# Kernel tuning notes

Hardware: AMD Instinct MI355X
Metric: run time of the kernel (lower is better)

## Reference

```python
import jax, jax.numpy as jnp
import numpy as np

E, D, H, N = 600000, 128, 256, 50000
LN_EPS = 1e-5


def layer_norm(x, g, b):
    mu = jnp.mean(x, axis=-1, keepdims=True)
    var = jnp.var(x, axis=-1, keepdims=True)
    return (x - mu) * jax.lax.rsqrt(var + LN_EPS) * g + b


def setup_inputs() -> dict:
    key = jax.random.key(0)
    ks = jax.random.split(key, 8)
    edges = jax.random.normal(ks[0], (E, D), dtype=jnp.float32)
    edges_index = jax.random.randint(ks[1], (E,), 0, N, dtype=jnp.int64)
    # params (PyTorch Linear default-ish init scale)
    w1 = jax.random.normal(ks[2], (D, H), dtype=jnp.float32) * (1.0 / np.sqrt(D))
    b1 = jnp.zeros((H,), dtype=jnp.float32)
    w2 = jax.random.normal(ks[3], (H, H), dtype=jnp.float32) * (1.0 / np.sqrt(H))
    b2 = jnp.zeros((H,), dtype=jnp.float32)
    wg = jax.random.normal(ks[4], (H, 1), dtype=jnp.float32) * (1.0 / np.sqrt(H))
    bg = jnp.zeros((1,), dtype=jnp.float32)
    wo = jax.random.normal(ks[5], (H, D), dtype=jnp.float32) * (1.0 / np.sqrt(H))
    bo = jnp.zeros((D,), dtype=jnp.float32)
    return {
        "edges": edges, "edges_index": edges_index, "num_nodes": N,
        "ln1_g": jnp.ones((D,), jnp.float32), "ln1_b": jnp.zeros((D,), jnp.float32),
        "w1": w1, "b1": b1,
        "ln2_g": jnp.ones((H,), jnp.float32), "ln2_b": jnp.zeros((H,), jnp.float32),
        "w2": w2, "b2": b2,
        "wg": wg, "bg": bg,
        "wo": wo, "bo": bo,
    }


def reference(edges, edges_index, num_nodes, ln1_g, ln1_b, w1, b1, ln2_g, ln2_b, w2, b2, wg, bg, wo, bo):
    # edge MLP: LN -> Linear -> ELU -> LN -> Linear
    h = layer_norm(edges, ln1_g, ln1_b)
    h = jax.nn.elu(h @ w1 + b1)
    h = layer_norm(h, ln2_g, ln2_b)
    h = h @ w2 + b2                      # [E, H]
    # gated output projection
    gate = jax.nn.sigmoid(h @ wg + bg)   # [E, 1]
    out = (h @ wo + bo) * gate           # [E, D]
    # scatter_add over destination nodes
    res = jax.ops.segment_sum(out, edges_index, num_segments=num_nodes)  # [N, D]
    return res
```

## Files before the change

### kernel.cpp

```cpp
#include <hip/hip_runtime.h>
#include <hip/hip_bf16.h>

typedef unsigned short u16;
typedef unsigned int u32;
typedef __bf16 bf16x8 __attribute__((ext_vector_type(8)));
typedef float f32x4 __attribute__((ext_vector_type(4)));

#define D 128
#define H 256
#define TM 32
#define THREADS 256
#define LN_EPS 1e-5f

__device__ __forceinline__ u32 f2bf(float f) {
    union { float f; u32 u; } v; v.f = f;
    return (v.u + 0x7FFFu + ((v.u >> 16) & 1u)) >> 16;
}

__global__ void pack_weights(const float* __restrict__ w1,
                             const float* __restrict__ w2,
                             const float* __restrict__ wo,
                             u16* __restrict__ pw) {
    int tid = blockIdx.x * blockDim.x + threadIdx.x;
    const float* W; int K, NN, local;
    if (tid < 32768)       { W = w1; K = 128; NN = 256; local = tid; }
    else if (tid < 98304)  { W = w2; K = 256; NN = 256; local = tid - 32768; }
    else if (tid < 131072) { W = wo; K = 256; NN = 128; local = tid - 98304; }
    else return;
    int b = local >> 9, within = local & 511;
    int l = within >> 3, i = within & 7;
    int nbk = K >> 5;
    int n0 = (b / nbk) << 4, k0 = (b % nbk) << 5;
    int k = k0 + ((l >> 4) << 3) + i;
    int n = n0 + (l & 15);
    pw[tid] = (u16)f2bf(W[k * NN + n]);
}

__global__ void zero_out_kernel(float4* __restrict__ out, int n4) {
    int i = blockIdx.x * blockDim.x + threadIdx.x;
    if (i < n4) out[i] = float4{0.f, 0.f, 0.f, 0.f};
}

__global__ __launch_bounds__(THREADS, 3) void fused_edge_kernel(
    const float* __restrict__ edges, const int* __restrict__ eidx,
    const float* __restrict__ ln1_g, const float* __restrict__ ln1_b,
    const float* __restrict__ b1,
    const float* __restrict__ ln2_g, const float* __restrict__ ln2_b,
    const float* __restrict__ b2,
    const float* __restrict__ wg, const float* __restrict__ bg,
    const float* __restrict__ bo,
    const u16* __restrict__ pw1, const u16* __restrict__ pw2,
    const u16* __restrict__ pwo,
    float* __restrict__ out, int E)
{
    __shared__ u16 sH[TM * H];
    __shared__ float sRedS[4][TM];
    __shared__ float sRedQ[4][TM];
    __shared__ float sMu[TM], sRs[TM], sGate[TM];
    __shared__ int   sIdx[TM];
    u16* sA = sH;

    const int t    = threadIdx.x;
    const int lane = t & 63;
    const int wave = t >> 6;
    const int lr   = lane & 15;
    const int lg   = lane >> 4;
    const int e0   = blockIdx.x * TM;

    if (t < TM) sIdx[t] = (e0 + t < E) ? eidx[e0 + t] : 0;

    {
        const int row = t >> 3;
        const int c8  = t & 7;
        const int er  = min(e0 + row, E - 1);
        const float* src = edges + (size_t)er * D + c8 * 16;
        float x[16];
        #pragma unroll
        for (int i = 0; i < 4; ++i) {
            float4 v = reinterpret_cast<const float4*>(src)[i];
            x[i*4+0]=v.x; x[i*4+1]=v.y; x[i*4+2]=v.z; x[i*4+3]=v.w;
        }
        float s = 0.f, sq = 0.f;
        #pragma unroll
        for (int i = 0; i < 16; ++i) { s += x[i]; sq += x[i]*x[i]; }
        s  += __shfl_xor(s, 1);  s  += __shfl_xor(s, 2);  s  += __shfl_xor(s, 4);
        sq += __shfl_xor(sq, 1); sq += __shfl_xor(sq, 2); sq += __shfl_xor(sq, 4);
        const float mu  = s * (1.0f / D);
        const float var = sq * (1.0f / D) - mu * mu;
        const float rs  = rsqrtf(var + LN_EPS);
        #pragma unroll
        for (int i = 0; i < 2; ++i) {
            u32 p[4];
            #pragma unroll
            for (int j = 0; j < 4; ++j) {
                int c0 = c8*16 + i*8 + j*2;
                float y0 = (x[i*8+j*2+0] - mu) * rs * ln1_g[c0+0] + ln1_b[c0+0];
                float y1 = (x[i*8+j*2+1] - mu) * rs * ln1_g[c0+1] + ln1_b[c0+1];
                p[j] = f2bf(y0) | (f2bf(y1) << 16);
            }
            int idx = (row * D + c8*16 + i*8) ^ ((row & 7) << 3);
            *reinterpret_cast<uint4*>(&sA[idx]) = uint4{p[0], p[1], p[2], p[3]};
        }
    }
    __syncthreads();

    f32x4 acc[2][4];
    #pragma unroll
    for (int a = 0; a < 2; ++a)
        #pragma unroll
        for (int b = 0; b < 4; ++b) acc[a][b] = f32x4{0.f,0.f,0.f,0.f};

    #pragma unroll
    for (int ks = 0; ks < 4; ++ks) {
        bf16x8 af[2];
        #pragma unroll
        for (int mt = 0; mt < 2; ++mt) {
            int row = mt*16 + lr;
            int idx = (row * D + ks*32 + lg*8) ^ ((row & 7) << 3);
            af[mt] = *reinterpret_cast<const bf16x8*>(&sA[idx]);
        }
        bf16x8 bv[4];
        #pragma unroll
        for (int nt = 0; nt < 4; ++nt) {
            int ctile = wave*4 + nt;
            int blk = ctile * 4 + ks;
            bv[nt] = *reinterpret_cast<const bf16x8*>(pw1 + blk*512 + lane*8);
        }
        #pragma unroll
        for (int mt = 0; mt < 2; ++mt)
            #pragma unroll
            for (int nt = 0; nt < 4; ++nt)
                acc[mt][nt] = __builtin_amdgcn_mfma_f32_16x16x32_bf16(af[mt], bv[nt], acc[mt][nt], 0, 0, 0);
    }

    float b1v[4];
    #pragma unroll
    for (int nt = 0; nt < 4; ++nt) b1v[nt] = b1[wave*64 + nt*16 + lr];
    float ps[2][4], pq[2][4];
    #pragma unroll
    for (int mt = 0; mt < 2; ++mt)
        #pragma unroll
        for (int r = 0; r < 4; ++r) { ps[mt][r] = 0.f; pq[mt][r] = 0.f; }
    #pragma unroll
    for (int mt = 0; mt < 2; ++mt)
        #pragma unroll
        for (int nt = 0; nt < 4; ++nt)
            #pragma unroll
            for (int r = 0; r < 4; ++r) {
                float x = acc[mt][nt][r] + b1v[nt];
                x = x > 0.f ? x : (__expf(x) - 1.f);
                acc[mt][nt][r] = x;
                ps[mt][r] += x;
                pq[mt][r] += x * x;
            }
    #pragma unroll
    for (int mt = 0; mt < 2; ++mt)
        #pragma unroll
        for (int r = 0; r < 4; ++r) {
            float s = ps[mt][r], q = pq[mt][r];
            s += __shfl_xor(s, 1); s += __shfl_xor(s, 2); s += __shfl_xor(s, 4); s += __shfl_xor(s, 8);
            q += __shfl_xor(q, 1); q += __shfl_xor(q, 2); q += __shfl_xor(q, 4); q += __shfl_xor(q, 8);
            ps[mt][r] = s; pq[mt][r] = q;
        }
    if (lr == 0) {
        #pragma unroll
        for (int mt = 0; mt < 2; ++mt)
            #pragma unroll
            for (int r = 0; r < 4; ++r) {
                int row = mt*16 + lg*4 + r;
                sRedS[wave][row] = ps[mt][r];
                sRedQ[wave][row] = pq[mt][r];
            }
    }
    __syncthreads();
    if (t < TM) {
        float S = sRedS[0][t] + sRedS[1][t] + sRedS[2][t] + sRedS[3][t];
        float Q = sRedQ[0][t] + sRedQ[1][t] + sRedQ[2][t] + sRedQ[3][t];
        float mu  = S * (1.0f / H);
        float var = Q * (1.0f / H) - mu * mu;
        sMu[t] = mu;
        sRs[t] = rsqrtf(var + LN_EPS);
    }
    __syncthreads();

    {
        float g2v[4], bt2[4];
        #pragma unroll
        for (int nt = 0; nt < 4; ++nt) {
            g2v[nt] = ln2_g[wave*64 + nt*16 + lr];
            bt2[nt] = ln2_b[wave*64 + nt*16 + lr];
        }
        #pragma unroll
        for (int mt = 0; mt < 2; ++mt)
            #pragma unroll
            for (int r = 0; r < 4; ++r) {
                int row = mt*16 + lg*4 + r;
                float mu = sMu[row], rs = sRs[row];
                #pragma unroll
                for (int nt = 0; nt < 4; ++nt) {
                    int col = wave*64 + nt*16 + lr;
                    float h = (acc[mt][nt][r] - mu) * rs * g2v[nt] + bt2[nt];
                    int idx = (row * H + col) ^ ((row & 7) << 3);
                    sH[idx] = (u16)f2bf(h);
                }
            }
    }
    __syncthreads();

    #pragma unroll
    for (int a = 0; a < 2; ++a)
        #pragma unroll
        for (int b = 0; b < 4; ++b) acc[a][b] = f32x4{0.f,0.f,0.f,0.f};

    #pragma unroll
    for (int ks = 0; ks < 8; ++ks) {
        bf16x8 af[2];
        #pragma unroll
        for (int mt = 0; mt < 2; ++mt) {
            int row = mt*16 + lr;
            int idx = (row * H + ks*32 + lg*8) ^ ((row & 7) << 3);
            af[mt] = *reinterpret_cast<const bf16x8*>(&sH[idx]);
        }
        bf16x8 bv[4];
        #pragma unroll
        for (int nt = 0; nt < 4; ++nt) {
            int ctile = wave*4 + nt;
            int blk = ctile * 8 + ks;
            bv[nt] = *reinterpret_cast<const bf16x8*>(pw2 + blk*512 + lane*8);
        }
        #pragma unroll
        for (int mt = 0; mt < 2; ++mt)
            #pragma unroll
            for (int nt = 0; nt < 4; ++nt)
                acc[mt][nt] = __builtin_amdgcn_mfma_f32_16x16x32_bf16(af[mt], bv[nt], acc[mt][nt], 0, 0, 0);
    }

    float b2v[4], wgv[4];
    #pragma unroll
    for (int nt = 0; nt < 4; ++nt) {
        b2v[nt] = b2[wave*64 + nt*16 + lr];
        wgv[nt] = wg[wave*64 + nt*16 + lr];
    }
    float pg[2][4];
    #pragma unroll
    for (int mt = 0; mt < 2; ++mt)
        #pragma unroll
        for (int r = 0; r < 4; ++r) pg[mt][r] = 0.f;
    #pragma unroll
    for (int mt = 0; mt < 2; ++mt)
        #pragma unroll
        for (int nt = 0; nt < 4; ++nt)
            #pragma unroll
            for (int r = 0; r < 4; ++r) {
                float h2 = acc[mt][nt][r] + b2v[nt];
                acc[mt][nt][r] = h2;
                pg[mt][r] += h2 * wgv[nt];
            }
    #pragma unroll
    for (int mt = 0; mt < 2; ++mt)
        #pragma unroll
        for (int r = 0; r < 4; ++r) {
            float s = pg[mt][r];
            s += __shfl_xor(s, 1); s += __shfl_xor(s, 2); s += __shfl_xor(s, 4); s += __shfl_xor(s, 8);
            pg[mt][r] = s;
        }
    __syncthreads();
    #pragma unroll
    for (int mt = 0; mt < 2; ++mt)
        #pragma unroll
        for (int r = 0; r < 4; ++r) {
            int row = mt*16 + lg*4 + r;
            #pragma unroll
            for (int nt = 0; nt < 4; ++nt) {
                int col = wave*64 + nt*16 + lr;
                int idx = (row * H + col) ^ ((row & 7) << 3);
                sH[idx] = (u16)f2bf(acc[mt][nt][r]);
            }
        }
    if (lr == 0) {
        #pragma unroll
        for (int mt = 0; mt < 2; ++mt)
            #pragma unroll
            for (int r = 0; r < 4; ++r)
                sRedS[wave][mt*16 + lg*4 + r] = pg[mt][r];
    }
    __syncthreads();
    if (t < TM) {
        float z = sRedS[0][t] + sRedS[1][t] + sRedS[2][t] + sRedS[3][t] + bg[0];
        sGate[t] = 1.0f / (1.0f + __expf(-z));
    }
    __syncthreads();

    f32x4 acc3[2][2];
    #pragma unroll
    for (int a = 0; a < 2; ++a)
        #pragma unroll
        for (int b = 0; b < 2; ++b) acc3[a][b] = f32x4{0.f,0.f,0.f,0.f};

    #pragma unroll
    for (int ks = 0; ks < 8; ++ks) {
        bf16x8 af[2];
        #pragma unroll
        for (int mt = 0; mt < 2; ++mt) {
            int row = mt*16 + lr;
            int idx = (row * H + ks*32 + lg*8) ^ ((row & 7) << 3);
            af[mt] = *reinterpret_cast<const bf16x8*>(&sH[idx]);
        }
        bf16x8 bv[2];
        #pragma unroll
        for (int nt = 0; nt < 2; ++nt) {
            int ctile = wave*2 + nt;
            int blk = ctile * 8 + ks;
            bv[nt] = *reinterpret_cast<const bf16x8*>(pwo + blk*512 + lane*8);
        }
        #pragma unroll
        for (int mt = 0; mt < 2; ++mt)
            #pragma unroll
            for (int nt = 0; nt < 2; ++nt)
                acc3[mt][nt] = __builtin_amdgcn_mfma_f32_16x16x32_bf16(af[mt], bv[nt], acc3[mt][nt], 0, 0, 0);
    }

    float bov[2];
    #pragma unroll
    for (int nt = 0; nt < 2; ++nt) bov[nt] = bo[wave*32 + nt*16 + lr];
    #pragma unroll
    for (int mt = 0; mt < 2; ++mt)
        #pragma unroll
        for (int r = 0; r < 4; ++r) {
            int row = mt*16 + lg*4 + r;
            if (e0 + row < E) {
                int node = sIdx[row];
                float gt = sGate[row];
                float* dst = out + (size_t)node * D;
                #pragma unroll
                for (int nt = 0; nt < 2; ++nt) {
                    int col = wave*32 + nt*16 + lr;
                    float v = (acc3[mt][nt][r] + bov[nt]) * gt;
                    unsafeAtomicAdd(dst + col, v);
                }
            }
        }
}

extern "C" void kernel_launch(void* const* d_in, const int* in_sizes, int n_in,
                              void* d_out, int out_size, void* d_ws, size_t ws_size,
                              hipStream_t stream) {
    const float* edges = (const float*)d_in[0];
    const int*   eidx  = (const int*)d_in[1];
    const float* ln1_g = (const float*)d_in[3];
    const float* ln1_b = (const float*)d_in[4];
    const float* w1    = (const float*)d_in[5];
    const float* b1    = (const float*)d_in[6];
    const float* ln2_g = (const float*)d_in[7];
    const float* ln2_b = (const float*)d_in[8];
    const float* w2    = (const float*)d_in[9];
    const float* b2    = (const float*)d_in[10];
    const float* wg    = (const float*)d_in[11];
    const float* bg    = (const float*)d_in[12];
    const float* wo    = (const float*)d_in[13];
    const float* bo    = (const float*)d_in[14];
    float* out = (float*)d_out;
    const int E = in_sizes[0] / D;

    u16* pw1 = (u16*)d_ws;
    u16* pw2 = pw1 + 32768;
    u16* pwo = pw1 + 98304;

    pack_weights<<<512, 256, 0, stream>>>(w1, w2, wo, pw1);
    int n4 = out_size / 4;
    zero_out_kernel<<<(n4 + 255) / 256, 256, 0, stream>>>((float4*)d_out, n4);
    fused_edge_kernel<<<(E + TM - 1) / TM, THREADS, 0, stream>>>(
        edges, eidx, ln1_g, ln1_b, b1, ln2_g, ln2_b, b2, wg, bg, bo,
        pw1, pw2, pwo, out, E);
}
```

Before: 444.6 us.

## Replace atomic scatter-add with CSR sort and per-node gather reduction

When the workspace is large enough, edges are bucketed by destination node: a histogram, a three-stage prefix scan and a placement kernel build a CSR order. The fused edge kernel then writes per-edge outputs to a workspace buffer, and a gather kernel sums each node's edges with plain stores instead of float atomics. The aim is to remove atomic contention and the output zeroing pass. The cost is about 300 MB of extra writes and reads for the per-edge buffer plus several small launches. The change also swaps hand-written bf16 rounding for native __bf16 casts and uses expm1f for ELU.

```diff
diff --git a/kernel.cpp b/kernel.cpp
--- a/kernel.cpp
+++ b/kernel.cpp
@@ -1,8 +1,6 @@
 #include <hip/hip_runtime.h>
 #include <hip/hip_bf16.h>
 
-typedef unsigned short u16;
-typedef unsigned int u32;
 typedef __bf16 bf16x8 __attribute__((ext_vector_type(8)));
 typedef float f32x4 __attribute__((ext_vector_type(4)));
 
@@ -11,16 +9,12 @@
 #define TM 32
 #define THREADS 256
 #define LN_EPS 1e-5f
-
-__device__ __forceinline__ u32 f2bf(float f) {
-    union { float f; u32 u; } v; v.f = f;
-    return (v.u + 0x7FFFu + ((v.u >> 16) & 1u)) >> 16;
-}
+#define NSCAN 50176
 
 __global__ void pack_weights(const float* __restrict__ w1,
                              const float* __restrict__ w2,
                              const float* __restrict__ wo,
-                             u16* __restrict__ pw) {
+                             __bf16* __restrict__ pw) {
     int tid = blockIdx.x * blockDim.x + threadIdx.x;
     const float* W; int K, NN, local;
     if (tid < 32768)       { W = w1; K = 128; NN = 256; local = tid; }
@@ -33,12 +27,89 @@
     int n0 = (b / nbk) << 4, k0 = (b % nbk) << 5;
     int k = k0 + ((l >> 4) << 3) + i;
     int n = n0 + (l & 15);
-    pw[tid] = (u16)f2bf(W[k * NN + n]);
+    pw[tid] = (__bf16)W[k * NN + n];
 }
 
 __global__ void zero_out_kernel(float4* __restrict__ out, int n4) {
     int i = blockIdx.x * blockDim.x + threadIdx.x;
     if (i < n4) out[i] = float4{0.f, 0.f, 0.f, 0.f};
+}
+
+__global__ void csr_zero_counts(int* __restrict__ counts) {
+    int i = blockIdx.x * blockDim.x + threadIdx.x;
+    if (i < NSCAN) counts[i] = 0;
+}
+
+__global__ void csr_hist(const int* __restrict__ eidx, int* __restrict__ counts,
+                         int* __restrict__ pos, int E) {
+    int e = blockIdx.x * blockDim.x + threadIdx.x;
+    if (e < E) pos[e] = atomicAdd(&counts[eidx[e]], 1);
+}
+
+__global__ void csr_scan1(const int* __restrict__ counts, int* __restrict__ offs,
+                          int* __restrict__ bsum) {
+    __shared__ int wsum[4];
+    int tid = threadIdx.x, blk = blockIdx.x;
+    int base = blk * 1024 + tid * 4;
+    int c0 = counts[base], c1 = counts[base+1], c2 = counts[base+2], c3 = counts[base+3];
+    int tot = c0 + c1 + c2 + c3;
+    int lane = tid & 63, wv = tid >> 6;
+    int inc = tot;
+    #pragma unroll
+    for (int d = 1; d < 64; d <<= 1) {
+        int v = __shfl_up(inc, d);
+        if (lane >= d) inc += v;
+    }
+    if (lane == 63) wsum[wv] = inc;
+    __syncthreads();
+    int wbase = 0;
+    for (int w = 0; w < wv; ++w) wbase += wsum[w];
+    int excl = wbase + inc - tot;
+    offs[base]   = excl;
+    offs[base+1] = excl + c0;
+    offs[base+2] = excl + c0 + c1;
+    offs[base+3] = excl + c0 + c1 + c2;
+    if (tid == 255) bsum[blk] = wbase + inc;
+}
+
+__global__ void csr_scan2(int* __restrict__ bsum) {
+    int l = threadIdx.x;
+    int v = (l < 49) ? bsum[l] : 0;
+    int inc = v;
+    #pragma unroll
+    for (int d = 1; d < 64; d <<= 1) {
+        int u = __shfl_up(inc, d);
+        if (l >= d) inc += u;
+    }
+    if (l < 49) bsum[l] = inc - v;
+}
+
+__global__ void csr_scan3(int* __restrict__ offs, const int* __restrict__ bsum) {
+    int i = blockIdx.x * blockDim.x + threadIdx.x;
+    if (i < NSCAN) offs[i] += bsum[i >> 10];
+}
+
+__global__ void csr_place(const int* __restrict__ eidx, const int* __restrict__ offs,
+                          const int* __restrict__ pos, int* __restrict__ order, int E) {
+    int e = blockIdx.x * blockDim.x + threadIdx.x;
+    if (e < E) order[offs[eidx[e]] + pos[e]] = e;
+}
+
+__global__ __launch_bounds__(256) void gather_kernel(
+    const float* __restrict__ eout, const int* __restrict__ offs,
+    const int* __restrict__ order, float* __restrict__ out, int N) {
+    int wave = threadIdx.x >> 6, lane = threadIdx.x & 63;
+    int n = blockIdx.x * 4 + wave;
+    if (n >= N) return;
+    int beg = offs[n];
+    int end = offs[n + 1];
+    float ax = 0.f, ay = 0.f;
+    for (int j = beg; j < end; ++j) {
+        int e = order[j];
+        const float2 v = *reinterpret_cast<const float2*>(eout + (size_t)e * D + lane * 2);
+        ax += v.x; ay += v.y;
+    }
+    *reinterpret_cast<float2*>(out + (size_t)n * D + lane * 2) = float2{ax, ay};
 }
 
 __global__ __launch_bounds__(THREADS, 3) void fused_edge_kernel(
@@ -49,16 +120,19 @@
     const float* __restrict__ b2,
     const float* __restrict__ wg, const float* __restrict__ bg,
     const float* __restrict__ bo,
-    const u16* __restrict__ pw1, const u16* __restrict__ pw2,
-    const u16* __restrict__ pwo,
-    float* __restrict__ out, int E)
+    const __bf16* __restrict__ pw,
+    float* __restrict__ out, float* __restrict__ eout, int use_eout, int E)
 {
-    __shared__ u16 sH[TM * H];
+    __shared__ __bf16 sH[TM * H];
     __shared__ float sRedS[4][TM];
     __shared__ float sRedQ[4][TM];
     __shared__ float sMu[TM], sRs[TM], sGate[TM];
     __shared__ int   sIdx[TM];
-    u16* sA = sH;
+    __bf16* sA = sH;
+
+    const __bf16* pw1 = pw;
+    const __bf16* pw2 = pw + 32768;
+    const __bf16* pwo = pw + 98304;
 
     const int t    = threadIdx.x;
     const int lane = t & 63;
@@ -90,16 +164,14 @@
         const float rs  = rsqrtf(var + LN_EPS);
         #pragma unroll
         for (int i = 0; i < 2; ++i) {
-            u32 p[4];
-            #pragma unroll
-            for (int j = 0; j < 4; ++j) {
-                int c0 = c8*16 + i*8 + j*2;
-                float y0 = (x[i*8+j*2+0] - mu) * rs * ln1_g[c0+0] + ln1_b[c0+0];
-                float y1 = (x[i*8+j*2+1] - mu) * rs * ln1_g[c0+1] + ln1_b[c0+1];
-                p[j] = f2bf(y0) | (f2bf(y1) << 16);
+            bf16x8 yv;
+            #pragma unroll
+            for (int j = 0; j < 8; ++j) {
+                int c0 = c8*16 + i*8 + j;
+                yv[j] = (__bf16)((x[i*8+j] - mu) * rs * ln1_g[c0] + ln1_b[c0]);
             }
             int idx = (row * D + c8*16 + i*8) ^ ((row & 7) << 3);
-            *reinterpret_cast<uint4*>(&sA[idx]) = uint4{p[0], p[1], p[2], p[3]};
+            *reinterpret_cast<bf16x8*>(&sA[idx]) = yv;
         }
     }
     __syncthreads();
@@ -122,8 +194,7 @@
         bf16x8 bv[4];
         #pragma unroll
         for (int nt = 0; nt < 4; ++nt) {
-            int ctile = wave*4 + nt;
-            int blk = ctile * 4 + ks;
+            int blk = (wave*4 + nt) * 4 + ks;
             bv[nt] = *reinterpret_cast<const bf16x8*>(pw1 + blk*512 + lane*8);
         }
         #pragma unroll
@@ -136,40 +207,36 @@
     float b1v[4];
     #pragma unroll
     for (int nt = 0; nt < 4; ++nt) b1v[nt] = b1[wave*64 + nt*16 + lr];
-    float ps[2][4], pq[2][4];
-    #pragma unroll
-    for (int mt = 0; mt < 2; ++mt)
-        #pragma unroll
-        for (int r = 0; r < 4; ++r) { ps[mt][r] = 0.f; pq[mt][r] = 0.f; }
-    #pragma unroll
-    for (int mt = 0; mt < 2; ++mt)
-        #pragma unroll
-        for (int nt = 0; nt < 4; ++nt)
+    {
+        float ps[2][4], pq[2][4];
+        #pragma unroll
+        for (int mt = 0; mt < 2; ++mt)
+            #pragma unroll
+            for (int r = 0; r < 4; ++r) { ps[mt][r] = 0.f; pq[mt][r] = 0.f; }
+        #pragma unroll
+        for (int mt = 0; mt < 2; ++mt)
+            #pragma unroll
+            for (int nt = 0; nt < 4; ++nt)
+                #pragma unroll
+                for (int r = 0; r < 4; ++r) {
+                    float x = acc[mt][nt][r] + b1v[nt];
+                    x = x > 0.f ? x : expm1f(x);
+                    acc[mt][nt][r] = x;
+                    ps[mt][r] += x;
+                    pq[mt][r] += x * x;
+                }
+        #pragma unroll
+        for (int mt = 0; mt < 2; ++mt)
             #pragma unroll
             for (int r = 0; r < 4; ++r) {
-                float x = acc[mt][nt][r] + b1v[nt];
-                x = x > 0.f ? x : (__expf(x) - 1.f);
-                acc[mt][nt][r] = x;
-                ps[mt][r] += x;
-                pq[mt][r] += x * x;
-            }
-    #pragma unroll
-    for (int mt = 0; mt < 2; ++mt)
-        #pragma unroll
-        for (int r = 0; r < 4; ++r) {
-            float s = ps[mt][r], q = pq[mt][r];
-            s += __shfl_xor(s, 1); s += __shfl_xor(s, 2); s += __shfl_xor(s, 4); s += __shfl_xor(s, 8);
-            q += __shfl_xor(q, 1); q += __shfl_xor(q, 2); q += __shfl_xor(q, 4); q += __shfl_xor(q, 8);
-            ps[mt][r] = s; pq[mt][r] = q;
-        }
-    if (lr == 0) {
-        #pragma unroll
-        for (int mt = 0; mt < 2; ++mt)
-            #pragma unroll
-            for (int r = 0; r < 4; ++r) {
-                int row = mt*16 + lg*4 + r;
-                sRedS[wave][row] = ps[mt][r];
-                sRedQ[wave][row] = pq[mt][r];
+                float s = ps[mt][r], q = pq[mt][r];
+                s += __shfl_xor(s, 1); s += __shfl_xor(s, 2); s += __shfl_xor(s, 4); s += __shfl_xor(s, 8);
+                q += __shfl_xor(q, 1); q += __shfl_xor(q, 2); q += __shfl_xor(q, 4); q += __shfl_xor(q, 8);
+                if (lr == 0) {
+                    int row = mt*16 + lg*4 + r;
+                    sRedS[wave][row] = s;
+                    sRedQ[wave][row] = q;
+                }
             }
     }
     __syncthreads();
@@ -201,7 +268,7 @@
                     int col = wave*64 + nt*16 + lr;
                     float h = (acc[mt][nt][r] - mu) * rs * g2v[nt] + bt2[nt];
                     int idx = (row * H + col) ^ ((row & 7) << 3);
-                    sH[idx] = (u16)f2bf(h);
+                    sH[idx] = (__bf16)h;
                 }
             }
     }
@@ -224,8 +291,7 @@
         bf16x8 bv[4];
         #pragma unroll
         for (int nt = 0; nt < 4; ++nt) {
-            int ctile = wave*4 + nt;
-            int blk = ctile * 8 + ks;
+            int blk = (wave*4 + nt) * 8 + ks;
             bv[nt] = *reinterpret_cast<const bf16x8*>(pw2 + blk*512 + lane*8);
         }
         #pragma unroll
@@ -235,35 +301,37 @@
                 acc[mt][nt] = __builtin_amdgcn_mfma_f32_16x16x32_bf16(af[mt], bv[nt], acc[mt][nt], 0, 0, 0);
     }
 
-    float b2v[4], wgv[4];
-    #pragma unroll
-    for (int nt = 0; nt < 4; ++nt) {
-        b2v[nt] = b2[wave*64 + nt*16 + lr];
-        wgv[nt] = wg[wave*64 + nt*16 + lr];
-    }
     float pg[2][4];
-    #pragma unroll
-    for (int mt = 0; mt < 2; ++mt)
-        #pragma unroll
-        for (int r = 0; r < 4; ++r) pg[mt][r] = 0.f;
-    #pragma unroll
-    for (int mt = 0; mt < 2; ++mt)
-        #pragma unroll
-        for (int nt = 0; nt < 4; ++nt)
+    {
+        float b2v[4], wgv[4];
+        #pragma unroll
+        for (int nt = 0; nt < 4; ++nt) {
+            b2v[nt] = b2[wave*64 + nt*16 + lr];
+            wgv[nt] = wg[wave*64 + nt*16 + lr];
+        }
+        #pragma unroll
+        for (int mt = 0; mt < 2; ++mt)
+            #pragma unroll
+            for (int r = 0; r < 4; ++r) pg[mt][r] = 0.f;
+        #pragma unroll
+        for (int mt = 0; mt < 2; ++mt)
+            #pragma unroll
+            for (int nt = 0; nt < 4; ++nt)
+                #pragma unroll
+                for (int r = 0; r < 4; ++r) {
+                    float h2 = acc[mt][nt][r] + b2v[nt];
+                    acc[mt][nt][r] = h2;
+                    pg[mt][r] += h2 * wgv[nt];
+                }
+        #pragma unroll
+        for (int mt = 0; mt < 2; ++mt)
             #pragma unroll
             for (int r = 0; r < 4; ++r) {
-                float h2 = acc[mt][nt][r] + b2v[nt];
-                acc[mt][nt][r] = h2;
-                pg[mt][r] += h2 * wgv[nt];
+                float s = pg[mt][r];
+                s += __shfl_xor(s, 1); s += __shfl_xor(s, 2); s += __shfl_xor(s, 4); s += __shfl_xor(s, 8);
+                pg[mt][r] = s;
             }
-    #pragma unroll
-    for (int mt = 0; mt < 2; ++mt)
-        #pragma unroll
-        for (int r = 0; r < 4; ++r) {
-            float s = pg[mt][r];
-            s += __shfl_xor(s, 1); s += __shfl_xor(s, 2); s += __shfl_xor(s, 4); s += __shfl_xor(s, 8);
-            pg[mt][r] = s;
-        }
+    }
     __syncthreads();
     #pragma unroll
     for (int mt = 0; mt < 2; ++mt)
@@ -274,7 +342,7 @@
             for (int nt = 0; nt < 4; ++nt) {
                 int col = wave*64 + nt*16 + lr;
                 int idx = (row * H + col) ^ ((row & 7) << 3);
-                sH[idx] = (u16)f2bf(acc[mt][nt][r]);
+                sH[idx] = (__bf16)acc[mt][nt][r];
             }
         }
     if (lr == 0) {
@@ -309,8 +377,7 @@
         bf16x8 bv[2];
         #pragma unroll
         for (int nt = 0; nt < 2; ++nt) {
-            int ctile = wave*2 + nt;
-            int blk = ctile * 8 + ks;
+            int blk = (wave*2 + nt) * 8 + ks;
             bv[nt] = *reinterpret_cast<const bf16x8*>(pwo + blk*512 + lane*8);
         }
         #pragma unroll
@@ -320,26 +387,47 @@
                 acc3[mt][nt] = __builtin_amdgcn_mfma_f32_16x16x32_bf16(af[mt], bv[nt], acc3[mt][nt], 0, 0, 0);
     }
 
-    float bov[2];
-    #pragma unroll
-    for (int nt = 0; nt < 2; ++nt) bov[nt] = bo[wave*32 + nt*16 + lr];
-    #pragma unroll
-    for (int mt = 0; mt < 2; ++mt)
-        #pragma unroll
-        for (int r = 0; r < 4; ++r) {
-            int row = mt*16 + lg*4 + r;
-            if (e0 + row < E) {
-                int node = sIdx[row];
-                float gt = sGate[row];
-                float* dst = out + (size_t)node * D;
+    {
+        float bov[2];
+        #pragma unroll
+        for (int nt = 0; nt < 2; ++nt) bov[nt] = bo[wave*32 + nt*16 + lr];
+        if (use_eout) {
+            #pragma unroll
+            for (int mt = 0; mt < 2; ++mt)
                 #pragma unroll
-                for (int nt = 0; nt < 2; ++nt) {
-                    int col = wave*32 + nt*16 + lr;
-                    float v = (acc3[mt][nt][r] + bov[nt]) * gt;
-                    unsafeAtomicAdd(dst + col, v);
-                }
-            }
-        }
+                for (int r = 0; r < 4; ++r) {
+                    int row = mt*16 + lg*4 + r;
+                    int e = e0 + row;
+                    if (e < E) {
+                        float gt = sGate[row];
+                        float* dst = eout + (size_t)e * D;
+                        #pragma unroll
+                        for (int nt = 0; nt < 2; ++nt) {
+                            int col = wave*32 + nt*16 + lr;
+                            dst[col] = (acc3[mt][nt][r] + bov[nt]) * gt;
+                        }
+                    }
+                }
+        } else {
+            #pragma unroll
+            for (int mt = 0; mt < 2; ++mt)
+                #pragma unroll
+                for (int r = 0; r < 4; ++r) {
+                    int row = mt*16 + lg*4 + r;
+                    if (e0 + row < E) {
+                        int node = sIdx[row];
+                        float gt = sGate[row];
+                        float* dst = out + (size_t)node * D;
+                        #pragma unroll
+                        for (int nt = 0; nt < 2; ++nt) {
+                            int col = wave*32 + nt*16 + lr;
+                            float v = (acc3[mt][nt][r] + bov[nt]) * gt;
+                            unsafeAtomicAdd(dst + col, v);
+                        }
+                    }
+                }
+        }
+    }
 }
 
 extern "C" void kernel_launch(void* const* d_in, const int* in_sizes, int n_in,
@@ -361,15 +449,45 @@
     const float* bo    = (const float*)d_in[14];
     float* out = (float*)d_out;
     const int E = in_sizes[0] / D;
-
-    u16* pw1 = (u16*)d_ws;
-    u16* pw2 = pw1 + 32768;
-    u16* pwo = pw1 + 98304;
-
-    pack_weights<<<512, 256, 0, stream>>>(w1, w2, wo, pw1);
-    int n4 = out_size / 4;
-    zero_out_kernel<<<(n4 + 255) / 256, 256, 0, stream>>>((float4*)d_out, n4);
-    fused_edge_kernel<<<(E + TM - 1) / TM, THREADS, 0, stream>>>(
-        edges, eidx, ln1_g, ln1_b, b1, ln2_g, ln2_b, b2, wg, bg, bo,
-        pw1, pw2, pwo, out, E);
-}
+    const int N = out_size / D;
+
+    size_t eout_b  = (size_t)E * D * sizeof(float);
+    size_t pw_b    = 131072 * sizeof(__bf16);
+    size_t cnt_b   = (size_t)NSCAN * sizeof(int);
+    size_t offs_b  = (size_t)(NSCAN + 1) * sizeof(int);
+    size_t bsum_b  = 64 * sizeof(int);
+    size_t posord_b = (size_t)E * sizeof(int);
+    size_t need = eout_b + pw_b + cnt_b + offs_b + bsum_b + 2 * posord_b;
+
+    const int use_csr = (ws_size >= need) ? 1 : 0;
+
+    if (use_csr) {
+        float* eout  = (float*)d_ws;
+        __bf16* pw   = (__bf16*)((char*)d_ws + eout_b);
+        int* counts  = (int*)((char*)pw + pw_b);
+        int* offs    = (int*)((char*)counts + cnt_b);
+        int* bsum    = (int*)((char*)offs + offs_b);
+        int* pos     = (int*)((char*)bsum + bsum_b);
+        int* order   = (int*)((char*)pos + posord_b);
+
+        pack_weights<<<512, 256, 0, stream>>>(w1, w2, wo, pw);
+        csr_zero_counts<<<NSCAN / 256, 256, 0, stream>>>(counts);
+        csr_hist<<<(E + 255) / 256, 256, 0, stream>>>(eidx, counts, pos, E);
+        csr_scan1<<<49, 256, 0, stream>>>(counts, offs, bsum);
+        csr_scan2<<<1, 64, 0, stream>>>(bsum);
+        csr_scan3<<<NSCAN / 256, 256, 0, stream>>>(offs, bsum);
+        csr_place<<<(E + 255) / 256, 256, 0, stream>>>(eidx, offs, pos, order, E);
+        fused_edge_kernel<<<(E + TM - 1) / TM, THREADS, 0, stream>>>(
+            edges, eidx, ln1_g, ln1_b, b1, ln2_g, ln2_b, b2, wg, bg, bo,
+            pw, out, eout, 1, E);
+        gather_kernel<<<(N + 3) / 4, 256, 0, stream>>>(eout, offs, order, out, N);
+    } else {
+        __bf16* pw = (__bf16*)d_ws;
+        pack_weights<<<512, 256, 0, stream>>>(w1, w2, wo, pw);
+        int n4 = out_size / 4;
+        zero_out_kernel<<<(n4 + 255) / 256, 256, 0, stream>>>((float4*)d_out, n4);
+        fused_edge_kernel<<<(E + TM - 1) / TM, THREADS, 0, stream>>>(
+            edges, eidx, ln1_g, ln1_b, b1, ln2_g, ln2_b, b2, wg, bg, bo,
+            pw, out, nullptr, 0, E);
+    }
+}
```

Measured after the change: 538.0 us. 21.0% more time.
